# Performance work log

Measured on AMD Instinct MI355X. Metric: run time of the kernel, lower is better.

## Reference

```python
import jax, jax.numpy as jnp
import numpy as np

DIM = 1024
N_STATE = 64
T, B = 512, 32


def _xavier(key, shape):
    fan_out, fan_in = shape
    limit = np.sqrt(6.0 / (fan_in + fan_out)).astype(np.float32)
    return jax.random.uniform(key, shape, jnp.float32, -limit, limit)


def setup_inputs() -> dict:
    key = jax.random.key(0)
    ks = jax.random.split(key, 5)
    return {
        "x": jax.random.normal(ks[0], (T, B, DIM), jnp.float32),
        "S": jnp.zeros((B, N_STATE, N_STATE), jnp.float32),
        "W_k": _xavier(ks[1], (N_STATE, DIM)),
        "W_v": _xavier(ks[2], (N_STATE, DIM)),
        "W_q": _xavier(ks[3], (N_STATE, DIM)),
        "W_alpha": _xavier(ks[4], (N_STATE, DIM)),
        "d_alpha": jnp.full((N_STATE,), 0.1, jnp.float32),
        "b_alpha": jnp.full((N_STATE,), 2.0, jnp.float32),
    }


def reference(x, S, W_k, W_v, W_q, W_alpha, d_alpha, b_alpha):
    # Precompute all projections as batched GEMMs: [T,B,n_state]
    k = jnp.einsum("tbd,nd->tbn", x, W_k)
    v = jnp.einsum("tbd,nd->tbn", x, W_v)
    q = jnp.einsum("tbd,nd->tbn", x, W_q)
    ax = jnp.einsum("tbd,nd->tbn", x, W_alpha)

    def step(S, inp):
        k_t, v_t, q_t, ax_t = inp  # each [B, n_state]
        retrieved = jnp.einsum("bij,bj->bi", S, k_t)          # S @ k
        alpha = jax.nn.sigmoid(ax_t + d_alpha * retrieved + b_alpha)
        # S = alpha * S + (1 - alpha) * outer(v, k); alpha gates rows
        S_new = alpha[:, :, None] * S + (1.0 - alpha)[:, :, None] * (
            v_t[:, :, None] * k_t[:, None, :]
        )
        h = jnp.einsum("bij,bj->bi", S_new, q_t)              # S @ q
        out_t = h * jax.nn.silu(h)                             # self-gated output
        return S_new, out_t

    S_final, output = jax.lax.scan(step, S, (k, v, q, ax))
    return output, S_final
```

## Files before the change

### kernel.cpp

```cpp
#include <hip/hip_runtime.h>
#include <hip/hip_bf16.h>

#define T_STEPS 512
#define BATCH 32
#define NST 64
#define DIM 1024

typedef _Float16 f16x8 __attribute__((ext_vector_type(8)));
typedef _Float16 f16x4 __attribute__((ext_vector_type(4)));
typedef _Float16 f16x2 __attribute__((ext_vector_type(2)));
typedef float f32x4 __attribute__((ext_vector_type(4)));

__device__ __forceinline__ void gl_lds16(const void* g, void* l) {
  __builtin_amdgcn_global_load_lds(
      (const __attribute__((address_space(1))) void*)g,
      (__attribute__((address_space(3))) void*)l, 16, 0, 0);
}

__global__ __launch_bounds__(256) void wconv(
    const float* __restrict__ Wk, const float* __restrict__ Wv,
    const float* __restrict__ Wq, const float* __restrict__ Wa,
    _Float16* __restrict__ Wc) {
  const int n = blockIdx.x;
  const int g = n >> 6, r = n & 63;
  const float* W = (g == 0) ? Wk : (g == 1) ? Wq : (g == 2) ? Wv : Wa;
  float4 v = *(const float4*)(W + (size_t)r * DIM + threadIdx.x * 4);
  f16x4 h = {(_Float16)v.x, (_Float16)v.y, (_Float16)v.z, (_Float16)v.w};
  *(f16x4*)(Wc + (size_t)n * DIM + threadIdx.x * 4) = h;
}

__global__ __launch_bounds__(256) void proj_gemm(
    const float* __restrict__ x, const _Float16* __restrict__ Wc,
    _Float16* __restrict__ projh) {
  const int m0 = blockIdx.x * 64;
  const int n0 = blockIdx.y * 128;
  const int tid = threadIdx.x;
  const int lane = tid & 63, wv = tid >> 6;
  const int wm = wv >> 1, wn = wv & 1;
  const int fm = lane & 15, fq = lane >> 4;

  __shared__ __align__(16) _Float16 Al[64 * 40];
  __shared__ __align__(16) _Float16 Bl[2][128 * 32];

  const int bro = wv * 32 + (lane >> 2);
  const int bchunk = (lane & 3) ^ ((lane >> 3) & 3);
  const _Float16* gB = Wc + (size_t)(n0 + bro) * DIM + bchunk * 8;
  const int bl_off = bro * 32 + (lane & 3) * 8;

  const int arow = tid >> 2;
  const int acol = (tid & 3) * 8;
  const float* gA = x + (size_t)(m0 + arow) * DIM + acol;

  f32x4 acc[2][4];
#pragma unroll
  for (int mi = 0; mi < 2; ++mi)
#pragma unroll
    for (int ni = 0; ni < 4; ++ni) acc[mi][ni] = (f32x4){0.f, 0.f, 0.f, 0.f};

#define STAGE_B(buf, k0)                                       \
  {                                                            \
    _Pragma("unroll") for (int j = 0; j < 2; ++j)              \
        gl_lds16(gB + (size_t)j * 16 * DIM + (k0),             \
                 &Bl[buf][bl_off + j * 16 * 32]);              \
  }
  float4 xa, xb;
#define LOAD_A(k0)                          \
  {                                         \
    xa = *(const float4*)(gA + (k0));       \
    xb = *(const float4*)(gA + (k0) + 4);   \
  }

  STAGE_B(0, 0);
  LOAD_A(0);
  const int aswz = (fq ^ ((fm >> 1) & 3)) * 8;
  for (int kt = 0; kt < 32; ++kt) {
    __syncthreads();
    f16x8 ah;
    ah[0] = (_Float16)xa.x; ah[1] = (_Float16)xa.y;
    ah[2] = (_Float16)xa.z; ah[3] = (_Float16)xa.w;
    ah[4] = (_Float16)xb.x; ah[5] = (_Float16)xb.y;
    ah[6] = (_Float16)xb.z; ah[7] = (_Float16)xb.w;
    *(f16x8*)&Al[arow * 40 + acol] = ah;
    __syncthreads();
    if (kt + 1 < 32) {
      LOAD_A(kt * 32 + 32);
      STAGE_B((kt + 1) & 1, kt * 32 + 32);
    }
    f16x8 afr[2], bfr[4];
#pragma unroll
    for (int mi = 0; mi < 2; ++mi)
      afr[mi] = *(const f16x8*)&Al[(wm * 32 + mi * 16 + fm) * 40 + fq * 8];
#pragma unroll
    for (int ni = 0; ni < 4; ++ni) {
      const int row = wn * 64 + ni * 16 + fm;
      bfr[ni] = *(const f16x8*)&Bl[kt & 1][row * 32 + aswz];
    }
#pragma unroll
    for (int mi = 0; mi < 2; ++mi)
#pragma unroll
      for (int ni = 0; ni < 4; ++ni)
        acc[mi][ni] =
            __builtin_amdgcn_mfma_f32_16x16x32_f16(afr[mi], bfr[ni], acc[mi][ni], 0, 0, 0);
  }
#undef STAGE_B
#undef LOAD_A

#pragma unroll
  for (int mi = 0; mi < 2; ++mi)
#pragma unroll
    for (int ni = 0; ni < 4; ++ni) {
      const int gcol = n0 + wn * 64 + ni * 16 + fm;
      const int pcol = gcol < 128 ? gcol
                     : (gcol < 192 ? 128 + 2 * (gcol - 128) : 129 + 2 * (gcol - 192));
#pragma unroll
      for (int r = 0; r < 4; ++r) {
        const int grow = m0 + wm * 32 + mi * 16 + fq * 4 + r;
        projh[(size_t)grow * 256 + pcol] = (_Float16)acc[mi][ni][r];
      }
    }
}

__device__ __forceinline__ float red16(float x) {
  int v = __builtin_amdgcn_update_dpp(0, __float_as_int(x), 0xB1, 0xF, 0xF, true);
  x += __int_as_float(v);
  v = __builtin_amdgcn_update_dpp(0, __float_as_int(x), 0x4E, 0xF, 0xF, true);
  x += __int_as_float(v);
  v = __builtin_amdgcn_update_dpp(0, __float_as_int(x), 0x124, 0xF, 0xF, true);
  x += __int_as_float(v);
  v = __builtin_amdgcn_update_dpp(0, __float_as_int(x), 0x128, 0xF, 0xF, true);
  x += __int_as_float(v);
  return x;
}

__global__ __launch_bounds__(256) void scan_kernel(
    const _Float16* __restrict__ projh, const float* __restrict__ S0,
    const float* __restrict__ d_alpha, const float* __restrict__ b_alpha,
    float* __restrict__ out, float* __restrict__ Sout) {
  const int b = blockIdx.x >> 2;
  const int rg = blockIdx.x & 3;
  const int tid = threadIdx.x;
  const int c = tid & 15;
  const int r = rg * 16 + (tid >> 4);
  const int j0 = c * 4;

  __shared__ __align__(16) _Float16 lbuf[2 * 2048];

  float s[4];
  {
    float4 v = *(const float4*)(S0 + ((size_t)b * NST + r) * NST + j0);
    s[0] = v.x; s[1] = v.y; s[2] = v.z; s[3] = v.w;
  }
  const float da = d_alpha[r];
  const float ba = b_alpha[r];

  const _Float16* gp = projh + (size_t)b * 256;
  const int lidx = (tid >> 5) * 256 + (tid & 31) * 8;
#define GADDR(ch) (gp + (size_t)((ch) * 8 + (tid >> 5)) * (BATCH * 256) + (tid & 31) * 8)

  float4 rA;
  rA = *(const float4*)GADDR(0); *(float4*)(lbuf + lidx) = rA;
  rA = *(const float4*)GADDR(1); *(float4*)(lbuf + 2048 + lidx) = rA;
  rA = *(const float4*)GADDR(2);
  __syncthreads();

  f16x4 kf[2], qf[2];
  f16x2 vaf[2];
#define PREF(tn)                                                           \
  {                                                                        \
    const int pp = (tn)&1;                                                 \
    const _Float16* Pn = lbuf + (((tn) >> 3) & 1) * 2048 + ((tn)&7) * 256; \
    kf[pp] = *(const f16x4*)(Pn + j0);                                     \
    qf[pp] = *(const f16x4*)(Pn + 64 + j0);                                \
    vaf[pp] = *(const f16x2*)(Pn + 128 + 2 * r);                           \
  }

  PREF(0);
  for (int ch = 0; ch < 64; ++ch) {
#pragma unroll
    for (int si = 0; si < 8; ++si) {
      const int t = ch * 8 + si;
      const int p = t & 1;
      if (t + 1 < T_STEPS) PREF(t + 1);

      const float k0 = (float)kf[p][0], k1 = (float)kf[p][1];
      const float k2 = (float)kf[p][2], k3 = (float)kf[p][3];
      const float q0 = (float)qf[p][0], q1 = (float)qf[p][1];
      const float q2 = (float)qf[p][2], q3 = (float)qf[p][3];
      const float vi = (float)vaf[p][0];
      const float axv = (float)vaf[p][1];

      const float pa = fmaf(s[0], k0, s[1] * k1);
      const float pb = fmaf(s[2], k2, s[3] * k3);
      const float rr = red16(pa + pb);

      float z = fmaf(da, rr, axv + ba);
      z = fminf(fmaxf(z, -30.f), 30.f);
      const float e = __expf(-z);
      const float al = __builtin_amdgcn_rcpf(1.f + e);
      const float cc = (e * vi) * al;

      s[0] = fmaf(al, s[0], cc * k0);
      s[1] = fmaf(al, s[1], cc * k1);
      s[2] = fmaf(al, s[2], cc * k2);
      s[3] = fmaf(al, s[3], cc * k3);
      const float ha = fmaf(s[0], q0, s[1] * q1);
      const float hb = fmaf(s[2], q2, s[3] * q3);
      const float h = red16(ha + hb);

      if (c == 0) {
        const float sg = __builtin_amdgcn_rcpf(1.f + __expf(-h));
        out[((size_t)t * BATCH + b) * NST + r] = h * h * sg;
      }
    }
    if (ch + 2 < 64) {
      __syncthreads();
      *(float4*)(lbuf + (ch & 1) * 2048 + lidx) = rA;
      if (ch + 3 < 64) rA = *(const float4*)GADDR(ch + 3);
      __syncthreads();
    }
  }
#undef PREF
#undef GADDR

  float4 o = {s[0], s[1], s[2], s[3]};
  *(float4*)(Sout + ((size_t)b * NST + r) * NST + j0) = o;
}

extern "C" void kernel_launch(void* const* d_in, const int* in_sizes, int n_in,
                              void* d_out, int out_size, void* d_ws, size_t ws_size,
                              hipStream_t stream) {
  const float* x  = (const float*)d_in[0];
  const float* S0 = (const float*)d_in[1];
  const float* Wk = (const float*)d_in[2];
  const float* Wv = (const float*)d_in[3];
  const float* Wq = (const float*)d_in[4];
  const float* Wa = (const float*)d_in[5];
  const float* da = (const float*)d_in[6];
  const float* ba = (const float*)d_in[7];

  float* out  = (float*)d_out;
  float* Sout = out + (size_t)T_STEPS * BATCH * NST;
  _Float16* projh = (_Float16*)d_ws;
  _Float16* Wc = (_Float16*)((char*)d_ws + (size_t)16384 * 256 * 2);

  wconv<<<256, 256, 0, stream>>>(Wk, Wv, Wq, Wa, Wc);
  dim3 ggrid(16384 / 64, 2);
  proj_gemm<<<ggrid, 256, 0, stream>>>(x, Wc, projh);
  scan_kernel<<<4 * BATCH, 256, 0, stream>>>(projh, S0, da, ba, out, Sout);
}
```

Before: 226.3 us.

## Split GEMM over K halves, widen N tile, and fuse scan reductions algebraically

The projection GEMM now splits the K dimension across the two grid columns instead of N, so each block computes all 256 outputs and x is read once per block, with A double-buffered. The two fp16 partial sums are added in the scan kernel while staging into an fp32 LDS buffer. The scan computes S·k, S·q and k·q in parallel from the old state and forms h = al·(S·q) + cc·(k·q), which removes the serialized second reduction after the state update. It also switches to exp2 with prescaled constants and deepens register prefetch. The cost is double the workspace traffic and extra fp16 rounding of the partial sums.

Result: no change. 228.0 us (+0.7%).

```diff
diff --git a/kernel.cpp b/kernel.cpp
--- a/kernel.cpp
+++ b/kernel.cpp
@@ -5,10 +5,10 @@
 #define BATCH 32
 #define NST 64
 #define DIM 1024
+#define LOG2E 1.44269504f
 
 typedef _Float16 f16x8 __attribute__((ext_vector_type(8)));
 typedef _Float16 f16x4 __attribute__((ext_vector_type(4)));
-typedef _Float16 f16x2 __attribute__((ext_vector_type(2)));
 typedef float f32x4 __attribute__((ext_vector_type(4)));
 
 __device__ __forceinline__ void gl_lds16(const void* g, void* l) {
@@ -31,91 +31,92 @@
 
 __global__ __launch_bounds__(256) void proj_gemm(
     const float* __restrict__ x, const _Float16* __restrict__ Wc,
-    _Float16* __restrict__ projh) {
+    _Float16* __restrict__ P) {
   const int m0 = blockIdx.x * 64;
-  const int n0 = blockIdx.y * 128;
+  const int kh = blockIdx.y;
+  const int kbase = kh * 512;
   const int tid = threadIdx.x;
   const int lane = tid & 63, wv = tid >> 6;
   const int wm = wv >> 1, wn = wv & 1;
   const int fm = lane & 15, fq = lane >> 4;
 
-  __shared__ __align__(16) _Float16 Al[64 * 40];
-  __shared__ __align__(16) _Float16 Bl[2][128 * 32];
-
-  const int bro = wv * 32 + (lane >> 2);
+  __shared__ __align__(16) _Float16 Al[2][64 * 40];
+  __shared__ __align__(16) _Float16 Bl[2][256 * 32];
+
+  f32x4 acc[2][8];
+#pragma unroll
+  for (int mi = 0; mi < 2; ++mi)
+#pragma unroll
+    for (int ni = 0; ni < 8; ++ni) acc[mi][ni] = (f32x4){0.f, 0.f, 0.f, 0.f};
+
   const int bchunk = (lane & 3) ^ ((lane >> 3) & 3);
-  const _Float16* gB = Wc + (size_t)(n0 + bro) * DIM + bchunk * 8;
-  const int bl_off = bro * 32 + (lane & 3) * 8;
+  const _Float16* gB = Wc + (size_t)(wv * 64 + (lane >> 2)) * DIM + kbase + bchunk * 8;
+  _Float16* lB = &Bl[0][0] + (size_t)wv * 64 * 32 + lane * 8;
 
   const int arow = tid >> 2;
   const int acol = (tid & 3) * 8;
-  const float* gA = x + (size_t)(m0 + arow) * DIM + acol;
-
-  f32x4 acc[2][4];
-#pragma unroll
-  for (int mi = 0; mi < 2; ++mi)
-#pragma unroll
-    for (int ni = 0; ni < 4; ++ni) acc[mi][ni] = (f32x4){0.f, 0.f, 0.f, 0.f};
-
-#define STAGE_B(buf, k0)                                       \
-  {                                                            \
-    _Pragma("unroll") for (int j = 0; j < 2; ++j)              \
-        gl_lds16(gB + (size_t)j * 16 * DIM + (k0),             \
-                 &Bl[buf][bl_off + j * 16 * 32]);              \
+  const float* gA = x + (size_t)(m0 + arow) * DIM + kbase + acol;
+
+#define STAGE_B(buf, koff)                                          \
+  {                                                                 \
+    _Pragma("unroll") for (int j = 0; j < 4; ++j)                   \
+        gl_lds16(gB + (size_t)j * 16 * DIM + (koff),                \
+                 lB + (size_t)(buf) * 8192 + j * 512);              \
   }
   float4 xa, xb;
-#define LOAD_A(k0)                          \
-  {                                         \
-    xa = *(const float4*)(gA + (k0));       \
-    xb = *(const float4*)(gA + (k0) + 4);   \
-  }
-
+#define LOAD_A(koff)                          \
+  {                                           \
+    xa = *(const float4*)(gA + (koff));       \
+    xb = *(const float4*)(gA + (koff) + 4);   \
+  }
+
+  LOAD_A(0);
   STAGE_B(0, 0);
-  LOAD_A(0);
-  const int aswz = (fq ^ ((fm >> 1) & 3)) * 8;
-  for (int kt = 0; kt < 32; ++kt) {
-    __syncthreads();
+  for (int kt = 0; kt < 16; ++kt) {
+    const int cur = kt & 1;
     f16x8 ah;
     ah[0] = (_Float16)xa.x; ah[1] = (_Float16)xa.y;
     ah[2] = (_Float16)xa.z; ah[3] = (_Float16)xa.w;
     ah[4] = (_Float16)xb.x; ah[5] = (_Float16)xb.y;
     ah[6] = (_Float16)xb.z; ah[7] = (_Float16)xb.w;
-    *(f16x8*)&Al[arow * 40 + acol] = ah;
+    *(f16x8*)&Al[cur][arow * 40 + acol] = ah;
     __syncthreads();
-    if (kt + 1 < 32) {
-      LOAD_A(kt * 32 + 32);
-      STAGE_B((kt + 1) & 1, kt * 32 + 32);
-    }
-    f16x8 afr[2], bfr[4];
+    if (kt + 1 < 16) {
+      LOAD_A((kt + 1) * 32);
+      STAGE_B(cur ^ 1, (kt + 1) * 32);
+    }
+    f16x8 afr[2], bfr[8];
 #pragma unroll
     for (int mi = 0; mi < 2; ++mi)
-      afr[mi] = *(const f16x8*)&Al[(wm * 32 + mi * 16 + fm) * 40 + fq * 8];
-#pragma unroll
-    for (int ni = 0; ni < 4; ++ni) {
-      const int row = wn * 64 + ni * 16 + fm;
-      bfr[ni] = *(const f16x8*)&Bl[kt & 1][row * 32 + aswz];
+      afr[mi] = *(const f16x8*)&Al[cur][(wm * 32 + mi * 16 + fm) * 40 + fq * 8];
+    const int slot = fq ^ ((fm >> 1) & 3);
+#pragma unroll
+    for (int ni = 0; ni < 8; ++ni) {
+      const int row = wn * 128 + ni * 16 + fm;
+      bfr[ni] = *(const f16x8*)&Bl[cur][row * 32 + slot * 8];
     }
 #pragma unroll
     for (int mi = 0; mi < 2; ++mi)
 #pragma unroll
-      for (int ni = 0; ni < 4; ++ni)
+      for (int ni = 0; ni < 8; ++ni)
         acc[mi][ni] =
             __builtin_amdgcn_mfma_f32_16x16x32_f16(afr[mi], bfr[ni], acc[mi][ni], 0, 0, 0);
   }
 #undef STAGE_B
 #undef LOAD_A
 
+  _Float16* Pout = P + (size_t)kh * 16384 * 256;
 #pragma unroll
   for (int mi = 0; mi < 2; ++mi)
 #pragma unroll
-    for (int ni = 0; ni < 4; ++ni) {
-      const int gcol = n0 + wn * 64 + ni * 16 + fm;
+    for (int ni = 0; ni < 8; ++ni) {
+      const int gcol = wn * 128 + ni * 16 + fm;
       const int pcol = gcol < 128 ? gcol
                      : (gcol < 192 ? 128 + 2 * (gcol - 128) : 129 + 2 * (gcol - 192));
 #pragma unroll
       for (int r = 0; r < 4; ++r) {
         const int grow = m0 + wm * 32 + mi * 16 + fq * 4 + r;
-        projh[(size_t)grow * 256 + pcol] = (_Float16)acc[mi][ni][r];
+        Pout[(size_t)grow * 256 + pcol] = (_Float16)acc[mi][ni][r];
       }
     }
 }
@@ -133,9 +134,10 @@
 }
 
 __global__ __launch_bounds__(256) void scan_kernel(
-    const _Float16* __restrict__ projh, const float* __restrict__ S0,
-    const float* __restrict__ d_alpha, const float* __restrict__ b_alpha,
-    float* __restrict__ out, float* __restrict__ Sout) {
+    const _Float16* __restrict__ P0, const _Float16* __restrict__ P1,
+    const float* __restrict__ S0, const float* __restrict__ d_alpha,
+    const float* __restrict__ b_alpha, float* __restrict__ out,
+    float* __restrict__ Sout) {
   const int b = blockIdx.x >> 2;
   const int rg = blockIdx.x & 3;
   const int tid = threadIdx.x;
@@ -143,7 +145,7 @@
   const int r = rg * 16 + (tid >> 4);
   const int j0 = c * 4;
 
-  __shared__ __align__(16) _Float16 lbuf[2 * 2048];
+  __shared__ __align__(16) float lbuf[2 * 2048];
 
   float s[4];
   {
@@ -152,50 +154,72 @@
   }
   const float da = d_alpha[r];
   const float ba = b_alpha[r];
-
-  const _Float16* gp = projh + (size_t)b * 256;
+  const float mda = -da * LOG2E;
+
   const int lidx = (tid >> 5) * 256 + (tid & 31) * 8;
-#define GADDR(ch) (gp + (size_t)((ch) * 8 + (tid >> 5)) * (BATCH * 256) + (tid & 31) * 8)
-
-  float4 rA;
-  rA = *(const float4*)GADDR(0); *(float4*)(lbuf + lidx) = rA;
-  rA = *(const float4*)GADDR(1); *(float4*)(lbuf + 2048 + lidx) = rA;
-  rA = *(const float4*)GADDR(2);
+#define GOFF(ch) (((size_t)((ch) * 8 + (tid >> 5)) * BATCH + b) * 256 + (tid & 31) * 8)
+
+  f16x8 rA0, rA1;
+#define CVWR(slot)                                                   \
+  {                                                                  \
+    float4 w0, w1;                                                   \
+    w0.x = (float)rA0[0] + (float)rA1[0];                            \
+    w0.y = (float)rA0[1] + (float)rA1[1];                            \
+    w0.z = (float)rA0[2] + (float)rA1[2];                            \
+    w0.w = (float)rA0[3] + (float)rA1[3];                            \
+    w1.x = (float)rA0[4] + (float)rA1[4];                            \
+    w1.y = (float)rA0[5] + (float)rA1[5];                            \
+    w1.z = (float)rA0[6] + (float)rA1[6];                            \
+    w1.w = (float)rA0[7] + (float)rA1[7];                            \
+    *(float4*)(lbuf + (slot) * 2048 + lidx) = w0;                    \
+    *(float4*)(lbuf + (slot) * 2048 + lidx + 4) = w1;                \
+  }
+
+  rA0 = *(const f16x8*)(P0 + GOFF(0)); rA1 = *(const f16x8*)(P1 + GOFF(0));
+  CVWR(0);
+  rA0 = *(const f16x8*)(P0 + GOFF(1)); rA1 = *(const f16x8*)(P1 + GOFF(1));
+  CVWR(1);
+  rA0 = *(const f16x8*)(P0 + GOFF(2)); rA1 = *(const f16x8*)(P1 + GOFF(2));
   __syncthreads();
 
-  f16x4 kf[2], qf[2];
-  f16x2 vaf[2];
-#define PREF(tn)                                                           \
-  {                                                                        \
-    const int pp = (tn)&1;                                                 \
-    const _Float16* Pn = lbuf + (((tn) >> 3) & 1) * 2048 + ((tn)&7) * 256; \
-    kf[pp] = *(const f16x4*)(Pn + j0);                                     \
-    qf[pp] = *(const f16x4*)(Pn + 64 + j0);                                \
-    vaf[pp] = *(const f16x2*)(Pn + 128 + 2 * r);                           \
+  float4 kf[4], qf[4];
+  float2 va[4];
+#define PREF(tn)                                                             \
+  {                                                                          \
+    const int pp = (tn) & 3;                                                 \
+    const float* Pn = lbuf + (((tn) >> 3) & 1) * 2048 + ((tn) & 7) * 256;    \
+    kf[pp] = *(const float4*)(Pn + j0);                                      \
+    qf[pp] = *(const float4*)(Pn + 64 + j0);                                 \
+    va[pp] = *(const float2*)(Pn + 128 + 2 * r);                             \
   }
 
   PREF(0);
+  PREF(1);
   for (int ch = 0; ch < 64; ++ch) {
 #pragma unroll
     for (int si = 0; si < 8; ++si) {
       const int t = ch * 8 + si;
-      const int p = t & 1;
-      if (t + 1 < T_STEPS) PREF(t + 1);
-
-      const float k0 = (float)kf[p][0], k1 = (float)kf[p][1];
-      const float k2 = (float)kf[p][2], k3 = (float)kf[p][3];
-      const float q0 = (float)qf[p][0], q1 = (float)qf[p][1];
-      const float q2 = (float)qf[p][2], q3 = (float)qf[p][3];
-      const float vi = (float)vaf[p][0];
-      const float axv = (float)vaf[p][1];
-
-      const float pa = fmaf(s[0], k0, s[1] * k1);
-      const float pb = fmaf(s[2], k2, s[3] * k3);
+      const int p = t & 3;
+      if (t + 2 < T_STEPS) PREF(t + 2);
+
+      const float k0 = kf[p].x, k1 = kf[p].y, k2 = kf[p].z, k3 = kf[p].w;
+      const float q0 = qf[p].x, q1 = qf[p].y, q2 = qf[p].z, q3 = qf[p].w;
+      const float vi = va[p].x;
+      const float zcv = (va[p].y + ba) * (-LOG2E);
+
+      float pa = fmaf(s[0], k0, s[1] * k1);
+      float pb = fmaf(s[2], k2, s[3] * k3);
+      float ua = fmaf(s[0], q0, s[1] * q1);
+      float ub = fmaf(s[2], q2, s[3] * q3);
+      float ka = fmaf(k0, q0, k1 * q1);
+      float kb = fmaf(k2, q2, k3 * q3);
       const float rr = red16(pa + pb);
-
-      float z = fmaf(da, rr, axv + ba);
-      z = fminf(fmaxf(z, -30.f), 30.f);
-      const float e = __expf(-z);
+      const float uu = red16(ua + ub);
+      const float kq = red16(ka + kb);
+
+      float tt = fmaf(rr, mda, zcv);
+      tt = fminf(fmaxf(tt, -45.f), 45.f);
+      const float e = exp2f(tt);
       const float al = __builtin_amdgcn_rcpf(1.f + e);
       const float cc = (e * vi) * al;
 
@@ -203,10 +227,8 @@
       s[1] = fmaf(al, s[1], cc * k1);
       s[2] = fmaf(al, s[2], cc * k2);
       s[3] = fmaf(al, s[3], cc * k3);
-      const float ha = fmaf(s[0], q0, s[1] * q1);
-      const float hb = fmaf(s[2], q2, s[3] * q3);
-      const float h = red16(ha + hb);
-
+
+      const float h = fmaf(al, uu, cc * kq);
       if (c == 0) {
         const float sg = __builtin_amdgcn_rcpf(1.f + __expf(-h));
         out[((size_t)t * BATCH + b) * NST + r] = h * h * sg;
@@ -214,13 +236,17 @@
     }
     if (ch + 2 < 64) {
       __syncthreads();
-      *(float4*)(lbuf + (ch & 1) * 2048 + lidx) = rA;
-      if (ch + 3 < 64) rA = *(const float4*)GADDR(ch + 3);
+      CVWR(ch & 1);
+      if (ch + 3 < 64) {
+        rA0 = *(const f16x8*)(P0 + GOFF(ch + 3));
+        rA1 = *(const f16x8*)(P1 + GOFF(ch + 3));
+      }
       __syncthreads();
     }
   }
 #undef PREF
-#undef GADDR
+#undef CVWR
+#undef GOFF
 
   float4 o = {s[0], s[1], s[2], s[3]};
   *(float4*)(Sout + ((size_t)b * NST + r) * NST + j0) = o;
@@ -240,11 +266,12 @@
 
   float* out  = (float*)d_out;
   float* Sout = out + (size_t)T_STEPS * BATCH * NST;
-  _Float16* projh = (_Float16*)d_ws;
-  _Float16* Wc = (_Float16*)((char*)d_ws + (size_t)16384 * 256 * 2);
+  _Float16* P = (_Float16*)d_ws;
+  _Float16* Wc = (_Float16*)((char*)d_ws + (size_t)16 * 1024 * 1024);
 
   wconv<<<256, 256, 0, stream>>>(Wk, Wv, Wq, Wa, Wc);
   dim3 ggrid(16384 / 64, 2);
-  proj_gemm<<<ggrid, 256, 0, stream>>>(x, Wc, projh);
-  scan_kernel<<<4 * BATCH, 256, 0, stream>>>(projh, S0, da, ba, out, Sout);
-}
+  proj_gemm<<<ggrid, 256, 0, stream>>>(x, Wc, P);
+  scan_kernel<<<4 * BATCH, 256, 0, stream>>>(P, P + (size_t)16384 * 256, S0, da, ba,
+                                             out, Sout);
+}
```
